# Kernel tuning notes

Measured on AMD Instinct MI355X. Metric: run time of the kernel, lower is better.

## Reference

```python
import jax, jax.numpy as jnp
import numpy as np

EPS = 1e-5  # torch BatchNorm2d default eps


def _conv1x1(x, W, b):
    # x: [B,C,H,W], W: [O,C], b: [O]
    return jnp.einsum('bchw,oc->bohw', x, W) + b[None, :, None, None]


def _bn_eval(y, gamma, beta, mean, var):
    inv = gamma / jnp.sqrt(var + EPS)
    return y * inv[None, :, None, None] + (beta - mean * inv)[None, :, None, None]


def setup_inputs() -> dict:
    key = jax.random.key(0)
    ks = jax.random.split(key, 12)
    B, C, H, W = 4, 256, 64, 64
    mid = C // 4  # k = 4
    sc_in = (2.0 / C) ** 0.5   # kaiming_normal fan_in = C for 1x1 conv
    sc_mid = (2.0 / mid) ** 0.5
    x = jax.random.normal(ks[0], (B, C, H, W), jnp.float32)
    Wf = jax.random.normal(ks[1], (mid, C), jnp.float32) * sc_in
    bf = jnp.zeros((mid,), jnp.float32)
    gamma_f = jnp.ones((mid,), jnp.float32)
    beta_f = jnp.zeros((mid,), jnp.float32)
    mean_f = jax.random.normal(ks[2], (mid,), jnp.float32) * 0.1
    var_f = jax.random.uniform(ks[3], (mid,), jnp.float32, 0.5, 1.5)
    Wg = jax.random.normal(ks[4], (mid, C), jnp.float32) * sc_in
    bg = jnp.zeros((mid,), jnp.float32)
    gamma_g = jnp.ones((mid,), jnp.float32)
    beta_g = jnp.zeros((mid,), jnp.float32)
    mean_g = jax.random.normal(ks[5], (mid,), jnp.float32) * 0.1
    var_g = jax.random.uniform(ks[6], (mid,), jnp.float32, 0.5, 1.5)
    Wh = jax.random.normal(ks[7], (mid, C), jnp.float32) * sc_in
    bh = jnp.zeros((mid,), jnp.float32)
    # v conv is constant-initialized to 0 in the original; use small random
    # weights so the attention branch contributes to the output under test.
    Wv = jax.random.normal(ks[8], (C, mid), jnp.float32) * sc_mid * 0.1
    bv = jnp.zeros((C,), jnp.float32)
    v0 = jax.random.normal(ks[9], (B, H * W, 1), jnp.float32)  # power-iter init
    return dict(x=x, Wf=Wf, bf=bf, gamma_f=gamma_f, beta_f=beta_f, mean_f=mean_f,
                var_f=var_f, Wg=Wg, bg=bg, gamma_g=gamma_g, beta_g=beta_g,
                mean_g=mean_g, var_g=var_g, Wh=Wh, bh=bh, Wv=Wv, bv=bv, v0=v0)


def reference(x, Wf, bf, gamma_f, beta_f, mean_f, var_f,
              Wg, bg, gamma_g, beta_g, mean_g, var_g,
              Wh, bh, Wv, bv, v0):
    B, C, H, W = x.shape
    mid = Wf.shape[0]
    HW = H * W
    f_x = jax.nn.relu(_bn_eval(_conv1x1(x, Wf, bf), gamma_f, beta_f, mean_f, var_f)).reshape(B, mid, HW)
    g_x = jax.nn.relu(_bn_eval(_conv1x1(x, Wg, bg), gamma_g, beta_g, mean_g, var_g)).reshape(B, mid, HW)
    h_x = _conv1x1(x, Wh, bh).reshape(B, mid, HW)
    # dense non-local correlation: [B, HW, HW]
    z = jnp.einsum('bcn,bcm->bnm', f_x, g_x)
    # power iteration (Ip=1) for spectral-norm estimate
    v = jnp.einsum('bnm,bmk->bnk', z, v0)          # [B,HW,1]
    v = v / jnp.linalg.norm(v[:, :, 0], axis=1)[:, None, None]
    s = jnp.einsum('bn,bnm,bm->b', v[:, :, 0], z, v[:, :, 0])[:, None, None]
    attn = z / s
    z2 = jnp.einsum('bnm,bcm->bcn', attn, h_x).reshape(B, mid, H, W)
    return _conv1x1(z2, Wv, bv) + x
```

## Files before the change

kernel.cpp:

```cpp
#include <hip/hip_runtime.h>

#define NB   4
#define CIN  256
#define MID  64
#define HW   4096
#define O3   192
#define KB_M 32

typedef __attribute__((ext_vector_type(8))) short bfrag8;
typedef __attribute__((ext_vector_type(4))) float facc4;

constexpr size_t OFF_FGHT  = 0;
constexpr size_t OFF_FHI   = 12582912;
constexpr size_t OFF_FLO   = 14680064;
constexpr size_t OFF_XHI   = 16777216;
constexpr size_t OFF_XLO   = 25165824;
constexpr size_t OFF_WHI   = 33554432;
constexpr size_t OFF_WLO   = 33652736;
constexpr size_t OFF_BEFF  = 33751040;
constexpr size_t OFF_W2HI  = 33752064;
constexpr size_t OFF_W2LO  = 33883136;
constexpr size_t OFF_MPART = 34014208;
constexpr size_t OFF_T     = 36111360;
constexpr size_t OFF_FGVU  = 36112384;
constexpr size_t OFF_NSQ   = 36114432;
constexpr size_t OFF_SVAL  = 36114688;

__device__ __forceinline__ unsigned short f2bf(float f) {
    union { float f; unsigned u; } v; v.f = f;
    unsigned r = v.u + 0x7FFF + ((v.u >> 16) & 1);
    return (unsigned short)(r >> 16);
}
__device__ __forceinline__ float bf2f(unsigned short h) {
    union { unsigned u; float f; } v; v.u = ((unsigned)h) << 16;
    return v.f;
}
__device__ __forceinline__ void split_bf(float v, unsigned short& hi, unsigned short& lo) {
    hi = f2bf(v);
    lo = f2bf(v - bf2f(hi));
}

__global__ void k_weff(const float* __restrict__ Wf, const float* __restrict__ bf,
                       const float* __restrict__ gf, const float* __restrict__ btf,
                       const float* __restrict__ mf, const float* __restrict__ vf,
                       const float* __restrict__ Wg, const float* __restrict__ bg,
                       const float* __restrict__ gg, const float* __restrict__ btg,
                       const float* __restrict__ mg, const float* __restrict__ vg,
                       const float* __restrict__ Wh, const float* __restrict__ bh,
                       unsigned short* __restrict__ whi, unsigned short* __restrict__ wlo,
                       float* __restrict__ beff) {
    const int o = blockIdx.x;
    const int c = threadIdx.x;
    float w, sh;
    if (o < 64) {
        float inv = gf[o] * rsqrtf(vf[o] + 1e-5f);
        w  = Wf[o * CIN + c] * inv;
        sh = bf[o] * inv + btf[o] - mf[o] * inv;
    } else if (o < 128) {
        int oo = o - 64;
        float inv = gg[oo] * rsqrtf(vg[oo] + 1e-5f);
        w  = Wg[oo * CIN + c] * inv;
        sh = bg[oo] * inv + btg[oo] - mg[oo] * inv;
    } else {
        int oo = o - 128;
        w  = Wh[oo * CIN + c];
        sh = bh[oo];
    }
    unsigned short hi, lo; split_bf(w, hi, lo);
    whi[o * CIN + c] = hi;
    wlo[o * CIN + c] = lo;
    if (c == 0) beff[o] = sh;
}

__launch_bounds__(256)
__global__ void k_xt(const float* __restrict__ x,
                     unsigned short* __restrict__ xhi, unsigned short* __restrict__ xlo) {
    __shared__ float tl[64][65];
    const int n0 = blockIdx.x * 64, c0 = blockIdx.y * 64, b = blockIdx.z;
    const int t = threadIdx.x;
    {
        const int c_r = t >> 2, nseg = t & 3;
        const float* src = x + ((size_t)(b * CIN + c0 + c_r)) * HW + n0 + nseg * 16;
        #pragma unroll
        for (int i = 0; i < 4; ++i) {
            float4 v = *(const float4*)(src + i * 4);
            tl[c_r][nseg * 16 + i * 4 + 0] = v.x;
            tl[c_r][nseg * 16 + i * 4 + 1] = v.y;
            tl[c_r][nseg * 16 + i * 4 + 2] = v.z;
            tl[c_r][nseg * 16 + i * 4 + 3] = v.w;
        }
    }
    __syncthreads();
    {
        const int n_r = t >> 2, cseg = t & 3;
        unsigned short th[16] __attribute__((aligned(16)));
        unsigned short tlo[16] __attribute__((aligned(16)));
        #pragma unroll
        for (int k = 0; k < 16; ++k)
            split_bf(tl[cseg * 16 + k][n_r], th[k], tlo[k]);
        const size_t base = ((size_t)(b * HW + n0 + n_r)) * CIN + c0 + cseg * 16;
        *(bfrag8*)(xhi + base)     = *(const bfrag8*)(th);
        *(bfrag8*)(xhi + base + 8) = *(const bfrag8*)(th + 8);
        *(bfrag8*)(xlo + base)     = *(const bfrag8*)(tlo);
        *(bfrag8*)(xlo + base + 8) = *(const bfrag8*)(tlo + 8);
    }
}

__launch_bounds__(256)
__global__ void k_fgh(const unsigned short* __restrict__ xhi, const unsigned short* __restrict__ xlo,
                      const unsigned short* __restrict__ whi_, const unsigned short* __restrict__ wlo_,
                      const float* __restrict__ beff, float* __restrict__ fghT,
                      unsigned short* __restrict__ fhi, unsigned short* __restrict__ flo) {
    __shared__ unsigned short xh[64][72], xl[64][72], wh[64][72], wl[64][72];
    const int n0 = blockIdx.x * 64;
    const int o0 = blockIdx.y * 64;
    const int b  = blockIdx.z;
    const int tid = threadIdx.x, l = tid & 63, w = tid >> 6;
    const int wo = w >> 1, wn = w & 1;
    const int lr = l & 15, lk = l >> 4;
    facc4 acc[2][2];
    #pragma unroll
    for (int i = 0; i < 2; ++i)
        #pragma unroll
        for (int j = 0; j < 2; ++j) acc[i][j] = (facc4){0.f, 0.f, 0.f, 0.f};

    const size_t xbase = ((size_t)(b * HW + n0)) * CIN;
    const size_t wbase = (size_t)o0 * CIN;

    for (int kc = 0; kc < 4; ++kc) {
        const int c0 = kc * 64;
        #pragma unroll
        for (int i = 0; i < 2; ++i) {
            int ch = tid + i * 256;
            int row = ch >> 3, cs = ch & 7;
            const size_t xsrc = xbase + (size_t)row * CIN + c0 + cs * 8;
            const size_t wsrc = wbase + (size_t)row * CIN + c0 + cs * 8;
            *(bfrag8*)&xh[row][cs * 8] = *(const bfrag8*)(xhi + xsrc);
            *(bfrag8*)&xl[row][cs * 8] = *(const bfrag8*)(xlo + xsrc);
            *(bfrag8*)&wh[row][cs * 8] = *(const bfrag8*)(whi_ + wsrc);
            *(bfrag8*)&wl[row][cs * 8] = *(const bfrag8*)(wlo_ + wsrc);
        }
        __syncthreads();
        #pragma unroll
        for (int ks = 0; ks < 2; ++ks) {
            bfrag8 ah[2], al[2], bh[2], bl[2];
            #pragma unroll
            for (int s = 0; s < 2; ++s) {
                ah[s] = *(const bfrag8*)&xh[wn * 32 + s * 16 + lr][ks * 32 + lk * 8];
                al[s] = *(const bfrag8*)&xl[wn * 32 + s * 16 + lr][ks * 32 + lk * 8];
                bh[s] = *(const bfrag8*)&wh[wo * 32 + s * 16 + lr][ks * 32 + lk * 8];
                bl[s] = *(const bfrag8*)&wl[wo * 32 + s * 16 + lr][ks * 32 + lk * 8];
            }
            #pragma unroll
            for (int sn = 0; sn < 2; ++sn)
                #pragma unroll
                for (int so = 0; so < 2; ++so) {
                    acc[sn][so] = __builtin_amdgcn_mfma_f32_16x16x32_bf16(ah[sn], bh[so], acc[sn][so], 0, 0, 0);
                    acc[sn][so] = __builtin_amdgcn_mfma_f32_16x16x32_bf16(ah[sn], bl[so], acc[sn][so], 0, 0, 0);
                    acc[sn][so] = __builtin_amdgcn_mfma_f32_16x16x32_bf16(al[sn], bh[so], acc[sn][so], 0, 0, 0);
                }
        }
        __syncthreads();
    }
    const bool rl = (o0 < 128);
    #pragma unroll
    for (int so = 0; so < 2; ++so) {
        const int o = o0 + wo * 32 + so * 16 + lr;
        const float bias = beff[o];
        #pragma unroll
        for (int sn = 0; sn < 2; ++sn)
            #pragma unroll
            for (int r = 0; r < 4; ++r) {
                const int n = n0 + wn * 32 + sn * 16 + lk * 4 + r;
                float v = acc[sn][so][r] + bias;
                if (rl) v = fmaxf(v, 0.0f);
                fghT[((size_t)(b * HW) + n) * O3 + o] = v;
                if (o0 == 0) {
                    unsigned short hi, lo; split_bf(v, hi, lo);
                    fhi[((size_t)(b * HW) + n) * MID + o] = hi;
                    flo[((size_t)(b * HW) + n) * MID + o] = lo;
                }
            }
    }
}

__global__ void k_t(const float* __restrict__ fghT, const float* __restrict__ v0,
                    float* __restrict__ t) {
    __shared__ float red[16][64];
    const int b = blockIdx.y, n0 = blockIdx.x * 128;
    const int tid = threadIdx.x, cq = tid & 15, ng = tid >> 4;
    float a[4] = {0.f, 0.f, 0.f, 0.f};
    for (int it = 0; it < 8; ++it) {
        const int n = n0 + ng + 16 * it;
        float4 gv = *(const float4*)(fghT + ((size_t)(b * HW) + n) * O3 + 64 + cq * 4);
        const float vv = v0[(size_t)b * HW + n];
        a[0] = fmaf(gv.x, vv, a[0]); a[1] = fmaf(gv.y, vv, a[1]);
        a[2] = fmaf(gv.z, vv, a[2]); a[3] = fmaf(gv.w, vv, a[3]);
    }
    #pragma unroll
    for (int i = 0; i < 4; ++i) red[ng][cq * 4 + i] = a[i];
    __syncthreads();
    if (tid < 64) {
        float s = 0.f;
        #pragma unroll
        for (int g = 0; g < 16; ++g) s += red[g][tid];
        atomicAdd(&t[b * MID + tid], s);
    }
}

__launch_bounds__(256)
__global__ void k_vfg(const float* __restrict__ fghT, const float* __restrict__ t,
                      float* __restrict__ fgvu, float* __restrict__ nsq) {
    __shared__ float ts[64];
    __shared__ float vuls[256];
    __shared__ float red2[8][128];
    __shared__ float rs[4];
    const int b = blockIdx.y, n0 = blockIdx.x * 256;
    const int tid = threadIdx.x;
    if (tid < 64) ts[tid] = t[b * MID + tid];
    __syncthreads();
    const int nl = tid >> 2, q = tid & 3;
    float mynsq = 0.f;
    for (int ps = 0; ps < 4; ++ps) {
        const int n = n0 + ps * 64 + nl;
        const float* p = fghT + ((size_t)(b * HW) + n) * O3 + q * 16;
        float a = 0.f;
        #pragma unroll
        for (int u = 0; u < 4; ++u) {
            float4 fv = *(const float4*)(p + u * 4);
            a = fmaf(fv.x, ts[q * 16 + u * 4 + 0], a);
            a = fmaf(fv.y, ts[q * 16 + u * 4 + 1], a);
            a = fmaf(fv.z, ts[q * 16 + u * 4 + 2], a);
            a = fmaf(fv.w, ts[q * 16 + u * 4 + 3], a);
        }
        a += __shfl_xor(a, 1);
        a += __shfl_xor(a, 2);
        if (q == 0) { vuls[ps * 64 + nl] = a; mynsq += a * a; }
    }
    {
        float s = mynsq;
        #pragma unroll
        for (int off = 32; off > 0; off >>= 1) s += __shfl_down(s, off);
        if ((tid & 63) == 0) rs[tid >> 6] = s;
        __syncthreads();
        if (tid == 0) atomicAdd(&nsq[b], rs[0] + rs[1] + rs[2] + rs[3]);
    }
    const int rq = tid & 31, ng2 = tid >> 5;
    float a2[4] = {0.f, 0.f, 0.f, 0.f};
    for (int it = 0; it < 32; ++it) {
        const int ni = ng2 + 8 * it;
        float4 fv = *(const float4*)(fghT + ((size_t)(b * HW) + n0 + ni) * O3 + rq * 4);
        const float vv = vuls[ni];
        a2[0] = fmaf(fv.x, vv, a2[0]); a2[1] = fmaf(fv.y, vv, a2[1]);
        a2[2] = fmaf(fv.z, vv, a2[2]); a2[3] = fmaf(fv.w, vv, a2[3]);
    }
    #pragma unroll
    for (int i = 0; i < 4; ++i) red2[ng2][rq * 4 + i] = a2[i];
    __syncthreads();
    if (tid < 128) {
        float s = 0.f;
        #pragma unroll
        for (int g = 0; g < 8; ++g) s += red2[g][tid];
        atomicAdd(&fgvu[b * 128 + tid], s);
    }
}

__global__ void k_s(const float* __restrict__ fgvu, const float* __restrict__ nsq,
                    float* __restrict__ sval) {
    const int b = blockIdx.x, c = threadIdx.x;
    float a = fgvu[b * 128 + c] * fgvu[b * 128 + 64 + c];
    #pragma unroll
    for (int off = 32; off > 0; off >>= 1) a += __shfl_down(a, off);
    if (c == 0) sval[b] = a / nsq[b];
}

__launch_bounds__(256)
__global__ void k_m(const float* __restrict__ fghT, float* __restrict__ mpart) {
    __shared__ float ghls[64][128];
    const int b = blockIdx.y, kb = blockIdx.x;
    const int tid = threadIdx.x, tc = tid & 15, tcp = tid >> 4;
    float acc[4][4];
    #pragma unroll
    for (int i = 0; i < 4; ++i)
        #pragma unroll
        for (int j = 0; j < 4; ++j) acc[i][j] = 0.f;
    for (int st = 0; st < 2; ++st) {
        const int nb = kb * 128 + st * 64;
        __syncthreads();
        #pragma unroll
        for (int i = 0; i < 8; ++i) {
            int ch = tid + i * 256;
            int row = ch >> 5, cs = ch & 31;
            *(float4*)&ghls[row][cs * 4] =
                *(const float4*)(fghT + ((size_t)(b * HW) + nb + row) * O3 + 64 + cs * 4);
        }
        __syncthreads();
        for (int nn = 0; nn < 64; ++nn) {
            float gv[4], hv[4];
            #pragma unroll
            for (int i = 0; i < 4; ++i) gv[i] = ghls[nn][tcp * 4 + i];
            #pragma unroll
            for (int j = 0; j < 4; ++j) hv[j] = ghls[nn][64 + tc * 4 + j];
            #pragma unroll
            for (int i = 0; i < 4; ++i)
                #pragma unroll
                for (int j = 0; j < 4; ++j) acc[i][j] = fmaf(gv[i], hv[j], acc[i][j]);
        }
    }
    #pragma unroll
    for (int i = 0; i < 4; ++i) {
        float4 v = make_float4(acc[i][0], acc[i][1], acc[i][2], acc[i][3]);
        *(float4*)(mpart + (((size_t)(b * KB_M + kb) * 64 + tcp * 4 + i) * 64 + tc * 4)) = v;
    }
}

__launch_bounds__(256)
__global__ void k_w2(const float* __restrict__ Wv, const float* __restrict__ mpart,
                     const float* __restrict__ sval,
                     unsigned short* __restrict__ w2hi, unsigned short* __restrict__ w2lo) {
    __shared__ float part[4][64];
    __shared__ float Mc[64];
    const int cp = blockIdx.x, b = blockIdx.y;
    const int tid = threadIdx.x;
    const int c = tid & 63, grp = tid >> 6;
    float s = 0.f;
    #pragma unroll
    for (int i = 0; i < 8; ++i) {
        const int kb = grp * 8 + i;
        s += mpart[((size_t)(b * KB_M + kb) * 64 + cp) * 64 + c];
    }
    part[grp][c] = s;
    __syncthreads();
    if (tid < 64) Mc[tid] = part[0][tid] + part[1][tid] + part[2][tid] + part[3][tid];
    __syncthreads();
    const float inv_s = 1.0f / sval[b];
    const int o = tid;
    float a = 0.f;
    #pragma unroll
    for (int u = 0; u < 16; ++u) {
        float4 wv4 = *(const float4*)(Wv + o * MID + u * 4);
        a = fmaf(wv4.x, Mc[u * 4 + 0], a);
        a = fmaf(wv4.y, Mc[u * 4 + 1], a);
        a = fmaf(wv4.z, Mc[u * 4 + 2], a);
        a = fmaf(wv4.w, Mc[u * 4 + 3], a);
    }
    unsigned short hi, lo; split_bf(a * inv_s, hi, lo);
    w2hi[((size_t)(b * CIN) + o) * MID + cp] = hi;
    w2lo[((size_t)(b * CIN) + o) * MID + cp] = lo;
}

__launch_bounds__(256)
__global__ void k_out(const float* __restrict__ x,
                      const unsigned short* __restrict__ fhi, const unsigned short* __restrict__ flo,
                      const unsigned short* __restrict__ w2hi, const unsigned short* __restrict__ w2lo,
                      const float* __restrict__ bv, float* __restrict__ out) {
    __shared__ unsigned short fh[64][72], fl[64][72], wh[64][72], wl[64][72];
    const int n0 = blockIdx.x * 64;
    const int o0 = blockIdx.y * 64;
    const int b  = blockIdx.z;
    const int tid = threadIdx.x, l = tid & 63, w = tid >> 6;
    const int wo = w >> 1, wn = w & 1;
    const int lr = l & 15, lk = l >> 4;
    #pragma unroll
    for (int i = 0; i < 2; ++i) {
        int ch = tid + i * 256;
        int row = ch >> 3, cs = ch & 7;
        const size_t fsrc = ((size_t)(b * HW) + n0 + row) * MID + cs * 8;
        const size_t wsrc = ((size_t)(b * CIN) + o0 + row) * MID + cs * 8;
        *(bfrag8*)&fh[row][cs * 8] = *(const bfrag8*)(fhi + fsrc);
        *(bfrag8*)&fl[row][cs * 8] = *(const bfrag8*)(flo + fsrc);
        *(bfrag8*)&wh[row][cs * 8] = *(const bfrag8*)(w2hi + wsrc);
        *(bfrag8*)&wl[row][cs * 8] = *(const bfrag8*)(w2lo + wsrc);
    }
    __syncthreads();
    facc4 acc[2][2];
    #pragma unroll
    for (int i = 0; i < 2; ++i)
        #pragma unroll
        for (int j = 0; j < 2; ++j) acc[i][j] = (facc4){0.f, 0.f, 0.f, 0.f};
    #pragma unroll
    for (int ks = 0; ks < 2; ++ks) {
        bfrag8 ah[2], al[2], bh[2], bl[2];
        #pragma unroll
        for (int s = 0; s < 2; ++s) {
            ah[s] = *(const bfrag8*)&wh[wo * 32 + s * 16 + lr][ks * 32 + lk * 8];
            al[s] = *(const bfrag8*)&wl[wo * 32 + s * 16 + lr][ks * 32 + lk * 8];
            bh[s] = *(const bfrag8*)&fh[wn * 32 + s * 16 + lr][ks * 32 + lk * 8];
            bl[s] = *(const bfrag8*)&fl[wn * 32 + s * 16 + lr][ks * 32 + lk * 8];
        }
        #pragma unroll
        for (int so = 0; so < 2; ++so)
            #pragma unroll
            for (int sn = 0; sn < 2; ++sn) {
                acc[so][sn] = __builtin_amdgcn_mfma_f32_16x16x32_bf16(ah[so], bh[sn], acc[so][sn], 0, 0, 0);
                acc[so][sn] = __builtin_amdgcn_mfma_f32_16x16x32_bf16(ah[so], bl[sn], acc[so][sn], 0, 0, 0);
                acc[so][sn] = __builtin_amdgcn_mfma_f32_16x16x32_bf16(al[so], bh[sn], acc[so][sn], 0, 0, 0);
            }
    }
    #pragma unroll
    for (int so = 0; so < 2; ++so)
        #pragma unroll
        for (int r = 0; r < 4; ++r) {
            const int o = o0 + wo * 32 + so * 16 + lk * 4 + r;
            const float bias = bv[o];
            #pragma unroll
            for (int sn = 0; sn < 2; ++sn) {
                const int n = n0 + wn * 32 + sn * 16 + lr;
                const size_t idx = ((size_t)(b * CIN) + o) * HW + n;
                out[idx] = x[idx] + bias + acc[so][sn][r];
            }
        }
}

extern "C" void kernel_launch(void* const* d_in, const int* in_sizes, int n_in,
                              void* d_out, int out_size, void* d_ws, size_t ws_size,
                              hipStream_t stream) {
    const float* x   = (const float*)d_in[0];
    const float* Wf  = (const float*)d_in[1];
    const float* bf  = (const float*)d_in[2];
    const float* gaf = (const float*)d_in[3];
    const float* bef = (const float*)d_in[4];
    const float* mef = (const float*)d_in[5];
    const float* vaf = (const float*)d_in[6];
    const float* Wg  = (const float*)d_in[7];
    const float* bg  = (const float*)d_in[8];
    const float* gag = (const float*)d_in[9];
    const float* beg = (const float*)d_in[10];
    const float* meg = (const float*)d_in[11];
    const float* vag = (const float*)d_in[12];
    const float* Wh  = (const float*)d_in[13];
    const float* bh  = (const float*)d_in[14];
    const float* Wv  = (const float*)d_in[15];
    const float* bv  = (const float*)d_in[16];
    const float* v0  = (const float*)d_in[17];
    float* out = (float*)d_out;
    char* ws = (char*)d_ws;

    float*          fghT = (float*)(ws + OFF_FGHT);
    unsigned short* fhi  = (unsigned short*)(ws + OFF_FHI);
    unsigned short* flo  = (unsigned short*)(ws + OFF_FLO);
    unsigned short* xhi  = (unsigned short*)(ws + OFF_XHI);
    unsigned short* xlo  = (unsigned short*)(ws + OFF_XLO);
    unsigned short* whi  = (unsigned short*)(ws + OFF_WHI);
    unsigned short* wlo  = (unsigned short*)(ws + OFF_WLO);
    float*          beff = (float*)(ws + OFF_BEFF);
    unsigned short* w2hi = (unsigned short*)(ws + OFF_W2HI);
    unsigned short* w2lo = (unsigned short*)(ws + OFF_W2LO);
    float*          mpart= (float*)(ws + OFF_MPART);
    float*          tvec = (float*)(ws + OFF_T);
    float*          fgvu = (float*)(ws + OFF_FGVU);
    float*          nsq  = (float*)(ws + OFF_NSQ);
    float*          sval = (float*)(ws + OFF_SVAL);

    hipMemsetAsync(tvec, 0, 3328, stream);

    k_weff<<<O3, CIN, 0, stream>>>(Wf, bf, gaf, bef, mef, vaf,
                                   Wg, bg, gag, beg, meg, vag,
                                   Wh, bh, whi, wlo, beff);
    k_xt  <<<dim3(HW / 64, CIN / 64, NB), 256, 0, stream>>>(x, xhi, xlo);
    k_fgh <<<dim3(HW / 64, O3 / 64, NB), 256, 0, stream>>>(xhi, xlo, whi, wlo, beff, fghT, fhi, flo);
    k_t   <<<dim3(32, NB), 256, 0, stream>>>(fghT, v0, tvec);
    k_m   <<<dim3(KB_M, NB), 256, 0, stream>>>(fghT, mpart);
    k_vfg <<<dim3(16, NB), 256, 0, stream>>>(fghT, tvec, fgvu, nsq);
    k_s   <<<NB, 64, 0, stream>>>(fgvu, nsq, sval);
    k_w2  <<<dim3(MID, NB), 256, 0, stream>>>(Wv, mpart, sval, w2hi, w2lo);
    k_out <<<dim3(HW / 64, CIN / 64, NB), 256, 0, stream>>>(x, fhi, flo, w2hi, w2lo, bv, out);
}
```

Measured before the change: 149.9 us.

## Fuse x transpose/split, f/g/h projection, t and M partials into one kernel

Removes the separate x transpose-and-split kernel by loading fp32 x directly in the projection kernel and splitting it to bf16 hi/lo on the fly. Each block now computes all 192 output channels for its 64-pixel tile, so x is read once instead of three times. The block then reduces g·v0 and the g^T h partial products in shared memory, which replaces the k_t and k_m kernels and drops the stored h... actually only f and g are written back, not h. The s computation is also merged into the W2 kernel, cutting launch count. In exchange the fused kernel uses more shared memory and registers per block, and the mpart buffer grows to 64 partials per batch that k_w2s must reduce.

```diff
diff --git a/kernel.cpp b/kernel.cpp
--- a/kernel.cpp
+++ b/kernel.cpp
@@ -4,27 +4,22 @@
 #define CIN  256
 #define MID  64
 #define HW   4096
-#define O3   192
-#define KB_M 32
 
 typedef __attribute__((ext_vector_type(8))) short bfrag8;
 typedef __attribute__((ext_vector_type(4))) float facc4;
 
 constexpr size_t OFF_FGHT  = 0;
-constexpr size_t OFF_FHI   = 12582912;
-constexpr size_t OFF_FLO   = 14680064;
-constexpr size_t OFF_XHI   = 16777216;
-constexpr size_t OFF_XLO   = 25165824;
-constexpr size_t OFF_WHI   = 33554432;
-constexpr size_t OFF_WLO   = 33652736;
-constexpr size_t OFF_BEFF  = 33751040;
-constexpr size_t OFF_W2HI  = 33752064;
-constexpr size_t OFF_W2LO  = 33883136;
-constexpr size_t OFF_MPART = 34014208;
-constexpr size_t OFF_T     = 36111360;
-constexpr size_t OFF_FGVU  = 36112384;
-constexpr size_t OFF_NSQ   = 36114432;
-constexpr size_t OFF_SVAL  = 36114688;
+constexpr size_t OFF_FHI   = 8388608;
+constexpr size_t OFF_FLO   = 10485760;
+constexpr size_t OFF_WHI   = 12582912;
+constexpr size_t OFF_WLO   = 12681216;
+constexpr size_t OFF_BEFF  = 12779520;
+constexpr size_t OFF_W2HI  = 12780544;
+constexpr size_t OFF_W2LO  = 12911616;
+constexpr size_t OFF_MPART = 13042688;
+constexpr size_t OFF_T     = 17236992;
+constexpr size_t OFF_FGVU  = 17238016;
+constexpr size_t OFF_NSQ   = 17240064;
 
 __device__ __forceinline__ unsigned short f2bf(float f) {
     union { float f; unsigned u; } v; v.f = f;
@@ -72,139 +67,153 @@
     if (c == 0) beff[o] = sh;
 }
 
-__launch_bounds__(256)
-__global__ void k_xt(const float* __restrict__ x,
-                     unsigned short* __restrict__ xhi, unsigned short* __restrict__ xlo) {
-    __shared__ float tl[64][65];
-    const int n0 = blockIdx.x * 64, c0 = blockIdx.y * 64, b = blockIdx.z;
-    const int t = threadIdx.x;
-    {
-        const int c_r = t >> 2, nseg = t & 3;
-        const float* src = x + ((size_t)(b * CIN + c0 + c_r)) * HW + n0 + nseg * 16;
-        #pragma unroll
-        for (int i = 0; i < 4; ++i) {
-            float4 v = *(const float4*)(src + i * 4);
-            tl[c_r][nseg * 16 + i * 4 + 0] = v.x;
-            tl[c_r][nseg * 16 + i * 4 + 1] = v.y;
-            tl[c_r][nseg * 16 + i * 4 + 2] = v.z;
-            tl[c_r][nseg * 16 + i * 4 + 3] = v.w;
-        }
-    }
-    __syncthreads();
-    {
-        const int n_r = t >> 2, cseg = t & 3;
-        unsigned short th[16] __attribute__((aligned(16)));
-        unsigned short tlo[16] __attribute__((aligned(16)));
-        #pragma unroll
-        for (int k = 0; k < 16; ++k)
-            split_bf(tl[cseg * 16 + k][n_r], th[k], tlo[k]);
-        const size_t base = ((size_t)(b * HW + n0 + n_r)) * CIN + c0 + cseg * 16;
-        *(bfrag8*)(xhi + base)     = *(const bfrag8*)(th);
-        *(bfrag8*)(xhi + base + 8) = *(const bfrag8*)(th + 8);
-        *(bfrag8*)(xlo + base)     = *(const bfrag8*)(tlo);
-        *(bfrag8*)(xlo + base + 8) = *(const bfrag8*)(tlo + 8);
-    }
-}
-
-__launch_bounds__(256)
-__global__ void k_fgh(const unsigned short* __restrict__ xhi, const unsigned short* __restrict__ xlo,
-                      const unsigned short* __restrict__ whi_, const unsigned short* __restrict__ wlo_,
-                      const float* __restrict__ beff, float* __restrict__ fghT,
-                      unsigned short* __restrict__ fhi, unsigned short* __restrict__ flo) {
-    __shared__ unsigned short xh[64][72], xl[64][72], wh[64][72], wl[64][72];
-    const int n0 = blockIdx.x * 64;
-    const int o0 = blockIdx.y * 64;
-    const int b  = blockIdx.z;
+__launch_bounds__(512)
+__global__ void k_fgh2(const float* __restrict__ x,
+                       const unsigned short* __restrict__ whi_g,
+                       const unsigned short* __restrict__ wlo_g,
+                       const float* __restrict__ beff,
+                       const float* __restrict__ v0,
+                       float* __restrict__ fghT,
+                       unsigned short* __restrict__ fhi,
+                       unsigned short* __restrict__ flo,
+                       float* __restrict__ tvec,
+                       float* __restrict__ mpart) {
+    __shared__ unsigned short xh[64][72], xl[64][72];
+    __shared__ char wbuf[2 * 192 * 72 * 2];
+    unsigned short (*wh)[72] = (unsigned short(*)[72])wbuf;
+    unsigned short (*wl)[72] = (unsigned short(*)[72])(wbuf + 192 * 72 * 2);
+
+    const int nb = blockIdx.x, b = blockIdx.y;
+    const int n0 = nb * 64;
     const int tid = threadIdx.x, l = tid & 63, w = tid >> 6;
     const int wo = w >> 1, wn = w & 1;
     const int lr = l & 15, lk = l >> 4;
-    facc4 acc[2][2];
+    facc4 acc[2][3];
     #pragma unroll
     for (int i = 0; i < 2; ++i)
         #pragma unroll
-        for (int j = 0; j < 2; ++j) acc[i][j] = (facc4){0.f, 0.f, 0.f, 0.f};
-
-    const size_t xbase = ((size_t)(b * HW + n0)) * CIN;
-    const size_t wbase = (size_t)o0 * CIN;
+        for (int j = 0; j < 3; ++j) acc[i][j] = (facc4){0.f, 0.f, 0.f, 0.f};
+
+    const int cr = tid >> 4, nq = tid & 15;
 
     for (int kc = 0; kc < 4; ++kc) {
         const int c0 = kc * 64;
-        #pragma unroll
-        for (int i = 0; i < 2; ++i) {
-            int ch = tid + i * 256;
-            int row = ch >> 3, cs = ch & 7;
-            const size_t xsrc = xbase + (size_t)row * CIN + c0 + cs * 8;
-            const size_t wsrc = wbase + (size_t)row * CIN + c0 + cs * 8;
-            *(bfrag8*)&xh[row][cs * 8] = *(const bfrag8*)(xhi + xsrc);
-            *(bfrag8*)&xl[row][cs * 8] = *(const bfrag8*)(xlo + xsrc);
-            *(bfrag8*)&wh[row][cs * 8] = *(const bfrag8*)(whi_ + wsrc);
-            *(bfrag8*)&wl[row][cs * 8] = *(const bfrag8*)(wlo_ + wsrc);
+        {
+            const float* xr = x + ((size_t)(b * CIN + c0 + cr * 2)) * HW + n0 + nq * 4;
+            float4 va = *(const float4*)xr;
+            float4 vb = *(const float4*)(xr + HW);
+            #pragma unroll
+            for (int i = 0; i < 4; ++i) {
+                float fa = (&va.x)[i], fb = (&vb.x)[i];
+                unsigned short ha, la, hb, lb;
+                split_bf(fa, ha, la);
+                split_bf(fb, hb, lb);
+                const int n = nq * 4 + i;
+                *(unsigned int*)&xh[n][cr * 2] = (unsigned int)ha | ((unsigned int)hb << 16);
+                *(unsigned int*)&xl[n][cr * 2] = (unsigned int)la | ((unsigned int)lb << 16);
+            }
+        }
+        {
+            #pragma unroll
+            for (int k = 0; k < 3; ++k) {
+                const int id = tid + k * 512;
+                const int orow = id >> 3, cs = id & 7;
+                *(bfrag8*)&wh[orow][cs * 8] = *(const bfrag8*)(whi_g + orow * CIN + c0 + cs * 8);
+                *(bfrag8*)&wl[orow][cs * 8] = *(const bfrag8*)(wlo_g + orow * CIN + c0 + cs * 8);
+            }
         }
         __syncthreads();
         #pragma unroll
         for (int ks = 0; ks < 2; ++ks) {
-            bfrag8 ah[2], al[2], bh[2], bl[2];
+            bfrag8 ah[2], al[2];
             #pragma unroll
             for (int s = 0; s < 2; ++s) {
                 ah[s] = *(const bfrag8*)&xh[wn * 32 + s * 16 + lr][ks * 32 + lk * 8];
                 al[s] = *(const bfrag8*)&xl[wn * 32 + s * 16 + lr][ks * 32 + lk * 8];
-                bh[s] = *(const bfrag8*)&wh[wo * 32 + s * 16 + lr][ks * 32 + lk * 8];
-                bl[s] = *(const bfrag8*)&wl[wo * 32 + s * 16 + lr][ks * 32 + lk * 8];
-            }
-            #pragma unroll
-            for (int sn = 0; sn < 2; ++sn)
+            }
+            #pragma unroll
+            for (int so = 0; so < 3; ++so) {
+                bfrag8 bh = *(const bfrag8*)&wh[wo * 48 + so * 16 + lr][ks * 32 + lk * 8];
+                bfrag8 bl = *(const bfrag8*)&wl[wo * 48 + so * 16 + lr][ks * 32 + lk * 8];
                 #pragma unroll
-                for (int so = 0; so < 2; ++so) {
-                    acc[sn][so] = __builtin_amdgcn_mfma_f32_16x16x32_bf16(ah[sn], bh[so], acc[sn][so], 0, 0, 0);
-                    acc[sn][so] = __builtin_amdgcn_mfma_f32_16x16x32_bf16(ah[sn], bl[so], acc[sn][so], 0, 0, 0);
-                    acc[sn][so] = __builtin_amdgcn_mfma_f32_16x16x32_bf16(al[sn], bh[so], acc[sn][so], 0, 0, 0);
+                for (int sn = 0; sn < 2; ++sn) {
+                    acc[sn][so] = __builtin_amdgcn_mfma_f32_16x16x32_bf16(ah[sn], bh, acc[sn][so], 0, 0, 0);
+                    acc[sn][so] = __builtin_amdgcn_mfma_f32_16x16x32_bf16(ah[sn], bl, acc[sn][so], 0, 0, 0);
+                    acc[sn][so] = __builtin_amdgcn_mfma_f32_16x16x32_bf16(al[sn], bh, acc[sn][so], 0, 0, 0);
                 }
+            }
         }
         __syncthreads();
     }
-    const bool rl = (o0 < 128);
-    #pragma unroll
-    for (int so = 0; so < 2; ++so) {
-        const int o = o0 + wo * 32 + so * 16 + lr;
+
+    float (*mls)[136]  = (float(*)[136])wbuf;
+    float (*tred)[64]  = (float(*)[64])(wbuf + 36864);
+    float* v0ls        = (float*)xh;
+
+    #pragma unroll
+    for (int so = 0; so < 3; ++so) {
+        const int o = wo * 48 + so * 16 + lr;
         const float bias = beff[o];
+        const bool rl = (o < 128);
         #pragma unroll
         for (int sn = 0; sn < 2; ++sn)
             #pragma unroll
             for (int r = 0; r < 4; ++r) {
-                const int n = n0 + wn * 32 + sn * 16 + lk * 4 + r;
+                const int nn = wn * 32 + sn * 16 + lk * 4 + r;
+                const int n = n0 + nn;
                 float v = acc[sn][so][r] + bias;
                 if (rl) v = fmaxf(v, 0.0f);
-                fghT[((size_t)(b * HW) + n) * O3 + o] = v;
-                if (o0 == 0) {
+                if (o < 128) fghT[((size_t)(b * HW) + n) * 128 + o] = v;
+                if (o < 64) {
                     unsigned short hi, lo; split_bf(v, hi, lo);
                     fhi[((size_t)(b * HW) + n) * MID + o] = hi;
                     flo[((size_t)(b * HW) + n) * MID + o] = lo;
                 }
-            }
-    }
-}
-
-__global__ void k_t(const float* __restrict__ fghT, const float* __restrict__ v0,
-                    float* __restrict__ t) {
-    __shared__ float red[16][64];
-    const int b = blockIdx.y, n0 = blockIdx.x * 128;
-    const int tid = threadIdx.x, cq = tid & 15, ng = tid >> 4;
-    float a[4] = {0.f, 0.f, 0.f, 0.f};
-    for (int it = 0; it < 8; ++it) {
-        const int n = n0 + ng + 16 * it;
-        float4 gv = *(const float4*)(fghT + ((size_t)(b * HW) + n) * O3 + 64 + cq * 4);
-        const float vv = v0[(size_t)b * HW + n];
-        a[0] = fmaf(gv.x, vv, a[0]); a[1] = fmaf(gv.y, vv, a[1]);
-        a[2] = fmaf(gv.z, vv, a[2]); a[3] = fmaf(gv.w, vv, a[3]);
-    }
-    #pragma unroll
-    for (int i = 0; i < 4; ++i) red[ng][cq * 4 + i] = a[i];
+                if (o >= 64) mls[nn][o - 64] = v;
+            }
+    }
+    if (tid < 64) v0ls[tid] = v0[(size_t)b * HW + n0 + tid];
+    __syncthreads();
+
+    {
+        const int c = tid & 63, ng = tid >> 6;
+        float tp = 0.f;
+        #pragma unroll
+        for (int i = 0; i < 8; ++i) {
+            const int nn = ng * 8 + i;
+            tp = fmaf(mls[nn][c], v0ls[nn], tp);
+        }
+        tred[ng][c] = tp;
+    }
+    {
+        const int tcp = tid >> 4, tc = tid & 15;
+        const int cp = tcp * 2, cc = tc * 4;
+        float macc[2][4];
+        #pragma unroll
+        for (int i = 0; i < 2; ++i)
+            #pragma unroll
+            for (int j = 0; j < 4; ++j) macc[i][j] = 0.f;
+        for (int nn = 0; nn < 64; ++nn) {
+            const float g0 = mls[nn][cp], g1 = mls[nn][cp + 1];
+            const float h0 = mls[nn][64 + cc + 0], h1 = mls[nn][64 + cc + 1];
+            const float h2 = mls[nn][64 + cc + 2], h3 = mls[nn][64 + cc + 3];
+            macc[0][0] = fmaf(g0, h0, macc[0][0]); macc[0][1] = fmaf(g0, h1, macc[0][1]);
+            macc[0][2] = fmaf(g0, h2, macc[0][2]); macc[0][3] = fmaf(g0, h3, macc[0][3]);
+            macc[1][0] = fmaf(g1, h0, macc[1][0]); macc[1][1] = fmaf(g1, h1, macc[1][1]);
+            macc[1][2] = fmaf(g1, h2, macc[1][2]); macc[1][3] = fmaf(g1, h3, macc[1][3]);
+        }
+        const size_t mpb = ((size_t)(b * 64 + nb) * 64) * 64;
+        *(float4*)&mpart[mpb + (size_t)(cp + 0) * 64 + cc] =
+            make_float4(macc[0][0], macc[0][1], macc[0][2], macc[0][3]);
+        *(float4*)&mpart[mpb + (size_t)(cp + 1) * 64 + cc] =
+            make_float4(macc[1][0], macc[1][1], macc[1][2], macc[1][3]);
+    }
     __syncthreads();
     if (tid < 64) {
         float s = 0.f;
         #pragma unroll
-        for (int g = 0; g < 16; ++g) s += red[g][tid];
-        atomicAdd(&t[b * MID + tid], s);
+        for (int g = 0; g < 8; ++g) s += tred[g][tid];
+        atomicAdd(&tvec[b * MID + tid], s);
     }
 }
 
@@ -223,7 +232,7 @@
     float mynsq = 0.f;
     for (int ps = 0; ps < 4; ++ps) {
         const int n = n0 + ps * 64 + nl;
-        const float* p = fghT + ((size_t)(b * HW) + n) * O3 + q * 16;
+        const float* p = fghT + ((size_t)(b * HW) + n) * 128 + q * 16;
         float a = 0.f;
         #pragma unroll
         for (int u = 0; u < 4; ++u) {
@@ -249,7 +258,7 @@
     float a2[4] = {0.f, 0.f, 0.f, 0.f};
     for (int it = 0; it < 32; ++it) {
         const int ni = ng2 + 8 * it;
-        float4 fv = *(const float4*)(fghT + ((size_t)(b * HW) + n0 + ni) * O3 + rq * 4);
+        float4 fv = *(const float4*)(fghT + ((size_t)(b * HW) + n0 + ni) * 128 + rq * 4);
         const float vv = vuls[ni];
         a2[0] = fmaf(fv.x, vv, a2[0]); a2[1] = fmaf(fv.y, vv, a2[1]);
         a2[2] = fmaf(fv.z, vv, a2[2]); a2[3] = fmaf(fv.w, vv, a2[3]);
@@ -265,88 +274,53 @@
     }
 }
 
-__global__ void k_s(const float* __restrict__ fgvu, const float* __restrict__ nsq,
-                    float* __restrict__ sval) {
-    const int b = blockIdx.x, c = threadIdx.x;
-    float a = fgvu[b * 128 + c] * fgvu[b * 128 + 64 + c];
-    #pragma unroll
-    for (int off = 32; off > 0; off >>= 1) a += __shfl_down(a, off);
-    if (c == 0) sval[b] = a / nsq[b];
-}
-
 __launch_bounds__(256)
-__global__ void k_m(const float* __restrict__ fghT, float* __restrict__ mpart) {
-    __shared__ float ghls[64][128];
-    const int b = blockIdx.y, kb = blockIdx.x;
-    const int tid = threadIdx.x, tc = tid & 15, tcp = tid >> 4;
-    float acc[4][4];
-    #pragma unroll
-    for (int i = 0; i < 4; ++i)
-        #pragma unroll
-        for (int j = 0; j < 4; ++j) acc[i][j] = 0.f;
-    for (int st = 0; st < 2; ++st) {
-        const int nb = kb * 128 + st * 64;
-        __syncthreads();
-        #pragma unroll
-        for (int i = 0; i < 8; ++i) {
-            int ch = tid + i * 256;
-            int row = ch >> 5, cs = ch & 31;
-            *(float4*)&ghls[row][cs * 4] =
-                *(const float4*)(fghT + ((size_t)(b * HW) + nb + row) * O3 + 64 + cs * 4);
-        }
-        __syncthreads();
-        for (int nn = 0; nn < 64; ++nn) {
-            float gv[4], hv[4];
-            #pragma unroll
-            for (int i = 0; i < 4; ++i) gv[i] = ghls[nn][tcp * 4 + i];
-            #pragma unroll
-            for (int j = 0; j < 4; ++j) hv[j] = ghls[nn][64 + tc * 4 + j];
-            #pragma unroll
-            for (int i = 0; i < 4; ++i)
-                #pragma unroll
-                for (int j = 0; j < 4; ++j) acc[i][j] = fmaf(gv[i], hv[j], acc[i][j]);
-        }
-    }
-    #pragma unroll
-    for (int i = 0; i < 4; ++i) {
-        float4 v = make_float4(acc[i][0], acc[i][1], acc[i][2], acc[i][3]);
-        *(float4*)(mpart + (((size_t)(b * KB_M + kb) * 64 + tcp * 4 + i) * 64 + tc * 4)) = v;
-    }
-}
-
-__launch_bounds__(256)
-__global__ void k_w2(const float* __restrict__ Wv, const float* __restrict__ mpart,
-                     const float* __restrict__ sval,
-                     unsigned short* __restrict__ w2hi, unsigned short* __restrict__ w2lo) {
-    __shared__ float part[4][64];
-    __shared__ float Mc[64];
-    const int cp = blockIdx.x, b = blockIdx.y;
+__global__ void k_w2s(const float* __restrict__ Wv, const float* __restrict__ mpart,
+                      const float* __restrict__ fgvu, const float* __restrict__ nsq,
+                      unsigned short* __restrict__ w2hi, unsigned short* __restrict__ w2lo) {
+    __shared__ float Mc[8][64];
+    __shared__ float svs;
+    const int cp0 = blockIdx.x * 8, b = blockIdx.y;
     const int tid = threadIdx.x;
-    const int c = tid & 63, grp = tid >> 6;
-    float s = 0.f;
-    #pragma unroll
-    for (int i = 0; i < 8; ++i) {
-        const int kb = grp * 8 + i;
-        s += mpart[((size_t)(b * KB_M + kb) * 64 + cp) * 64 + c];
-    }
-    part[grp][c] = s;
-    __syncthreads();
-    if (tid < 64) Mc[tid] = part[0][tid] + part[1][tid] + part[2][tid] + part[3][tid];
-    __syncthreads();
-    const float inv_s = 1.0f / sval[b];
+    {
+        const int c = tid & 63;
+        const int r0 = tid >> 6, r1 = r0 + 4;
+        float s0 = 0.f, s1 = 0.f;
+        for (int nb = 0; nb < 64; ++nb) {
+            const size_t base = ((size_t)(b * 64 + nb) * 64) * 64;
+            s0 += mpart[base + (size_t)(cp0 + r0) * 64 + c];
+            s1 += mpart[base + (size_t)(cp0 + r1) * 64 + c];
+        }
+        Mc[r0][c] = s0;
+        Mc[r1][c] = s1;
+    }
+    if (tid < 64) {
+        float a = fgvu[b * 128 + tid] * fgvu[b * 128 + 64 + tid];
+        #pragma unroll
+        for (int off = 32; off > 0; off >>= 1) a += __shfl_down(a, off);
+        if (tid == 0) svs = a / nsq[b];
+    }
+    __syncthreads();
+    const float inv_s = 1.0f / svs;
     const int o = tid;
-    float a = 0.f;
+    float wv[64];
     #pragma unroll
     for (int u = 0; u < 16; ++u) {
-        float4 wv4 = *(const float4*)(Wv + o * MID + u * 4);
-        a = fmaf(wv4.x, Mc[u * 4 + 0], a);
-        a = fmaf(wv4.y, Mc[u * 4 + 1], a);
-        a = fmaf(wv4.z, Mc[u * 4 + 2], a);
-        a = fmaf(wv4.w, Mc[u * 4 + 3], a);
-    }
-    unsigned short hi, lo; split_bf(a * inv_s, hi, lo);
-    w2hi[((size_t)(b * CIN) + o) * MID + cp] = hi;
-    w2lo[((size_t)(b * CIN) + o) * MID + cp] = lo;
+        float4 w4 = *(const float4*)(Wv + o * MID + u * 4);
+        wv[u * 4 + 0] = w4.x; wv[u * 4 + 1] = w4.y; wv[u * 4 + 2] = w4.z; wv[u * 4 + 3] = w4.w;
+    }
+    unsigned short rh[8] __attribute__((aligned(16)));
+    unsigned short rl[8] __attribute__((aligned(16)));
+    #pragma unroll
+    for (int j = 0; j < 8; ++j) {
+        float a = 0.f;
+        #pragma unroll
+        for (int c = 0; c < 64; ++c) a = fmaf(wv[c], Mc[j][c], a);
+        split_bf(a * inv_s, rh[j], rl[j]);
+    }
+    const size_t base = ((size_t)(b * CIN) + o) * MID + cp0;
+    *(bfrag8*)(w2hi + base) = *(const bfrag8*)rh;
+    *(bfrag8*)(w2lo + base) = *(const bfrag8*)rl;
 }
 
 __launch_bounds__(256)
@@ -439,8 +413,6 @@
     float*          fghT = (float*)(ws + OFF_FGHT);
     unsigned short* fhi  = (unsigned short*)(ws + OFF_FHI);
     unsigned short* flo  = (unsigned short*)(ws + OFF_FLO);
-    unsigned short* xhi  = (unsigned short*)(ws + OFF_XHI);
-    unsigned short* xlo  = (unsigned short*)(ws + OFF_XLO);
     unsigned short* whi  = (unsigned short*)(ws + OFF_WHI);
     unsigned short* wlo  = (unsigned short*)(ws + OFF_WLO);
     float*          beff = (float*)(ws + OFF_BEFF);
@@ -450,19 +422,15 @@
     float*          tvec = (float*)(ws + OFF_T);
     float*          fgvu = (float*)(ws + OFF_FGVU);
     float*          nsq  = (float*)(ws + OFF_NSQ);
-    float*          sval = (float*)(ws + OFF_SVAL);
 
     hipMemsetAsync(tvec, 0, 3328, stream);
 
-    k_weff<<<O3, CIN, 0, stream>>>(Wf, bf, gaf, bef, mef, vaf,
-                                   Wg, bg, gag, beg, meg, vag,
-                                   Wh, bh, whi, wlo, beff);
-    k_xt  <<<dim3(HW / 64, CIN / 64, NB), 256, 0, stream>>>(x, xhi, xlo);
-    k_fgh <<<dim3(HW / 64, O3 / 64, NB), 256, 0, stream>>>(xhi, xlo, whi, wlo, beff, fghT, fhi, flo);
-    k_t   <<<dim3(32, NB), 256, 0, stream>>>(fghT, v0, tvec);
-    k_m   <<<dim3(KB_M, NB), 256, 0, stream>>>(fghT, mpart);
+    k_weff<<<192, CIN, 0, stream>>>(Wf, bf, gaf, bef, mef, vaf,
+                                    Wg, bg, gag, beg, meg, vag,
+                                    Wh, bh, whi, wlo, beff);
+    k_fgh2<<<dim3(HW / 64, NB), 512, 0, stream>>>(x, whi, wlo, beff, v0,
+                                                  fghT, fhi, flo, tvec, mpart);
     k_vfg <<<dim3(16, NB), 256, 0, stream>>>(fghT, tvec, fgvu, nsq);
-    k_s   <<<NB, 64, 0, stream>>>(fgvu, nsq, sval);
-    k_w2  <<<dim3(MID, NB), 256, 0, stream>>>(Wv, mpart, sval, w2hi, w2lo);
+    k_w2s <<<dim3(8, NB), 256, 0, stream>>>(Wv, mpart, fgvu, nsq, w2hi, w2lo);
     k_out <<<dim3(HW / 64, CIN / 64, NB), 256, 0, stream>>>(x, fhi, flo, w2hi, w2lo, bv, out);
 }
```

After: 138.3 us. 7.7% less time.
